# Kernel tuning notes

Hardware: AMD Instinct MI355X
Metric: run time of the kernel (lower is better)

The kernel has to match this reference:

```python
import jax, jax.numpy as jnp
import numpy as np

N_NODES = 40000
N_EDGES = 640000
D_IN = 128
D_OUT = 128
ALPHA = 0.5   # real-valued complex alpha from init
Q = 0.25      # magnetic potential parameter


def setup_inputs() -> dict:
    key = jax.random.key(0)
    k = jax.random.split(key, 6)
    x = jax.random.normal(k[0], (N_NODES, D_IN), dtype=jnp.float32)
    edge_index = jax.random.randint(k[1], (2, N_EDGES), 0, N_NODES, dtype=jnp.int32)
    W1 = jax.random.normal(k[2], (D_IN, D_OUT), dtype=jnp.float32) * 0.05
    b1 = jax.random.normal(k[3], (D_OUT,), dtype=jnp.float32) * 0.05
    W2 = jax.random.normal(k[4], (D_IN, D_OUT), dtype=jnp.float32) * 0.05
    b2 = jax.random.normal(k[5], (D_OUT,), dtype=jnp.float32) * 0.05
    return {"x": x, "edge_index": edge_index, "W1": W1, "b1": b1, "W2": W2, "b2": b2}


def _magnet_spmm(x, edge_index, q):
    """y = H @ x where H = D_s^{-1/2} (A_s * exp(i*2*pi*q*(A - A^T))) D_s^{-1/2},
    A_s = 0.5*(A + A^T). Returns (y_real, y_imag); x is real (zero imag part)."""
    n = x.shape[0]
    row, col = edge_index[0], edge_index[1]
    e = row.shape[0]
    # detect whether the reverse edge (col,row) exists in the edge set
    keys = row * n + col
    rkeys = col * n + row
    sk = jnp.sort(keys)
    pos = jnp.searchsorted(sk, rkeys)
    has_rev = (pos < e) & (sk[jnp.clip(pos, 0, e - 1)] == rkeys)
    # symmetrize: each directed edge contributes 0.5 in both directions.
    # forward copy carries phase sign +1, reversed copy sign -1; phase is 0
    # when both directions exist (A - A^T = 0 there).
    r_all = jnp.concatenate([row, col])          # [2E]
    c_all = jnp.concatenate([col, row])
    sign = jnp.concatenate([jnp.ones((e,), x.dtype), -jnp.ones((e,), x.dtype)])
    hr = jnp.concatenate([has_rev, has_rev]).astype(x.dtype)
    theta = (2.0 * np.pi * q) * sign * (1.0 - hr)
    half = jnp.asarray(0.5, x.dtype)
    # symmetrized degree: deg[u] = sum_v A_s[u,v]
    deg = jax.ops.segment_sum(jnp.full((2 * e,), 0.5, x.dtype), r_all, num_segments=n)
    dinv = jnp.where(deg > 0, 1.0 / jnp.sqrt(deg), 0.0)
    scale = half * dinv[r_all] * dinv[c_all]
    val_re = scale * jnp.cos(theta)
    val_im = scale * jnp.sin(theta)
    xg = x[c_all]                                # [2E, D] gather
    y_re = jax.ops.segment_sum(val_re[:, None] * xg, r_all, num_segments=n)
    y_im = jax.ops.segment_sum(val_im[:, None] * xg, r_all, num_segments=n)
    return y_re, y_im


def reference(x, edge_index, W1, b1, W2, b2):
    y_re, y_im = _magnet_spmm(x, edge_index, Q)
    # alpha * lin1(y) + (1-alpha) * lin2(y), applied to real and imag parts
    out_re = ALPHA * (y_re @ W1 + b1) + (1.0 - ALPHA) * (y_re @ W2 + b2)
    out_im = ALPHA * (y_im @ W1 + b1) + (1.0 - ALPHA) * (y_im @ W2 + b2)
    return jnp.concatenate([out_re, out_im], axis=1)  # [N, 2*D_OUT]
```

## Files before the change

kernel.cpp:

```cpp
#include <hip/hip_runtime.h>
#include <math.h>

#define N_NODES 40000
#define D 128
#define NEDGE 640000
#define CAP 80
#define ZNB 64

__device__ __forceinline__ unsigned short bf16rn(float f) {
    unsigned u = __float_as_uint(f);
    unsigned r = u + 0x7FFFu + ((u >> 16) & 1u);
    return (unsigned short)(r >> 16);
}

__global__ __launch_bounds__(256) void zgemm_kernel(
    const float* __restrict__ x, const float* __restrict__ W1, const float* __restrict__ W2,
    unsigned short* __restrict__ z, int* __restrict__ cursorA, int* __restrict__ cursorB) {
    int tid = threadIdx.x;
    int gtid = blockIdx.x * 256 + tid;
    int gstride = gridDim.x * 256;
    for (int t = gtid; t < N_NODES; t += gstride) { cursorA[t] = 0; cursorB[t] = 0; }

    __shared__ float xl[ZNB][129];
    int node0 = blockIdx.x * ZNB;
    const float4* xs = (const float4*)(x + (size_t)node0 * D);
    for (int t = tid; t < ZNB * (D / 4); t += 256)
        *(float4*)&xl[t >> 5][(t & 31) * 4] = xs[t];
    __syncthreads();

    int ng = tid >> 4;
    int c8 = tid & 15;
    float acc[4][8];
    #pragma unroll
    for (int q = 0; q < 4; ++q)
        #pragma unroll
        for (int j = 0; j < 8; ++j) acc[q][j] = 0.f;

    const float4* W1v = (const float4*)W1;
    const float4* W2v = (const float4*)W2;
    #pragma unroll 2
    for (int k = 0; k < D; ++k) {
        float4 a1 = W1v[k * 32 + c8 * 2],     u1 = W1v[k * 32 + c8 * 2 + 1];
        float4 a2 = W2v[k * 32 + c8 * 2],     u2 = W2v[k * 32 + c8 * 2 + 1];
        float w[8];
        w[0] = 0.5f * (a1.x + a2.x); w[1] = 0.5f * (a1.y + a2.y);
        w[2] = 0.5f * (a1.z + a2.z); w[3] = 0.5f * (a1.w + a2.w);
        w[4] = 0.5f * (u1.x + u2.x); w[5] = 0.5f * (u1.y + u2.y);
        w[6] = 0.5f * (u1.z + u2.z); w[7] = 0.5f * (u1.w + u2.w);
        #pragma unroll
        for (int q = 0; q < 4; ++q) {
            float xv = xl[ng * 4 + q][k];
            #pragma unroll
            for (int j = 0; j < 8; ++j) acc[q][j] += xv * w[j];
        }
    }
    #pragma unroll
    for (int q = 0; q < 4; ++q) {
        int node = node0 + ng * 4 + q;
        ushort4 o1, o2;
        o1.x = bf16rn(acc[q][0]); o1.y = bf16rn(acc[q][1]);
        o1.z = bf16rn(acc[q][2]); o1.w = bf16rn(acc[q][3]);
        o2.x = bf16rn(acc[q][4]); o2.y = bf16rn(acc[q][5]);
        o2.z = bf16rn(acc[q][6]); o2.w = bf16rn(acc[q][7]);
        ushort4* zp = (ushort4*)(z + (size_t)node * D + c8 * 8);
        zp[0] = o1; zp[1] = o2;
    }
}

__global__ void expand_kernel(const int* __restrict__ row, const int* __restrict__ col,
                              int* __restrict__ cursorA, int* __restrict__ cursorB,
                              unsigned short* __restrict__ entries) {
    int i = blockIdx.x * blockDim.x + threadIdx.x;
    int gstride = gridDim.x * blockDim.x;
    for (int e = i; e < NEDGE; e += gstride) {
        int r = row[e], c = col[e];
        int p1 = atomicAdd(&cursorA[r], 1);
        if (p1 < CAP) entries[(size_t)r * CAP + p1] = (unsigned short)c;
        int p2 = atomicAdd(&cursorB[c], 1);
        if (p2 < CAP) entries[(size_t)c * CAP + (CAP - 1 - p2)] = (unsigned short)r;
    }
}

__global__ __launch_bounds__(256) void gather_kernel(
    const unsigned short* __restrict__ z, const unsigned short* __restrict__ entries,
    const int* __restrict__ cursorA, const int* __restrict__ cursorB,
    const float* __restrict__ b1, const float* __restrict__ b2,
    float* __restrict__ out) {
    __shared__ unsigned short rawlds[4][2][CAP];
    __shared__ uint2 slds[4][2][CAP];

    int tid = threadIdx.x;
    int wave = tid >> 6, half = (tid >> 5) & 1, l = tid & 31;
    int n = wave * 2 + half;
    int u = blockIdx.x * 8 + n;

    int cA = cursorA[u], cB = cursorB[u];
    int a = min(cA, CAP);
    int b = min(cB, CAP - a);
    int m = a + b;
    int cnt = cA + cB;
    float dinv_u = (cnt > 0) ? rsqrtf(0.5f * (float)cnt) : 0.f;
    const unsigned short* eb = entries + (size_t)u * CAP;
    int gap = CAP - m;

    for (int t = l; t < m; t += 32)
        rawlds[wave][half][t] = eb[t < a ? t : t + gap];
    __builtin_amdgcn_wave_barrier();

    for (int t = l; t < m; t += 32) {
        unsigned short src = rawlds[wave][half][t];
        bool d1 = (t >= a);
        int lo = d1 ? 0 : a, hi = d1 ? a : m;
        bool rev = false;
        for (int j = lo; j < hi; ++j)
            rev |= (rawlds[wave][half][j] == src);
        int cs = cursorA[src] + cursorB[src];
        float s = 0.5f * dinv_u * rsqrtf(0.5f * (float)max(cs, 1));
        unsigned flag = 0u;
        float sval;
        if (rev) { sval = s; flag = 0x10000u; }
        else     { sval = d1 ? -s : s; }
        slds[wave][half][t] = make_uint2((unsigned)src | flag, __float_as_uint(sval));
    }
    __builtin_amdgcn_wave_barrier();

    float4 accre = make_float4(0.f, 0.f, 0.f, 0.f);
    float4 accim = make_float4(0.f, 0.f, 0.f, 0.f);

    #pragma unroll 8
    for (int i = 0; i < m; ++i) {
        uint2 t = slds[wave][half][i];
        unsigned src = t.x & 0xFFFFu;
        float s = __uint_as_float(t.y);
        bool isre = (t.x & 0x10000u) != 0u;
        float fre = isre ? s : 0.f;
        float fim = isre ? 0.f : s;
        uint2 v = ((const uint2*)(z + (size_t)src * D))[l];
        float v0 = __uint_as_float(v.x << 16);
        float v1 = __uint_as_float(v.x & 0xFFFF0000u);
        float v2 = __uint_as_float(v.y << 16);
        float v3 = __uint_as_float(v.y & 0xFFFF0000u);
        accre.x += fre * v0; accre.y += fre * v1;
        accre.z += fre * v2; accre.w += fre * v3;
        accim.x += fim * v0; accim.y += fim * v1;
        accim.z += fim * v2; accim.w += fim * v3;
    }

    float4 ba = ((const float4*)b1)[l];
    float4 bb = ((const float4*)b2)[l];
    float4 bv = make_float4(0.5f * (ba.x + bb.x), 0.5f * (ba.y + bb.y),
                            0.5f * (ba.z + bb.z), 0.5f * (ba.w + bb.w));
    accre.x += bv.x; accre.y += bv.y; accre.z += bv.z; accre.w += bv.w;
    accim.x += bv.x; accim.y += bv.y; accim.z += bv.z; accim.w += bv.w;

    *(float4*)&out[(size_t)u * 256 + l * 4] = accre;
    *(float4*)&out[(size_t)u * 256 + 128 + l * 4] = accim;
}

extern "C" void kernel_launch(void* const* d_in, const int* in_sizes, int n_in,
                              void* d_out, int out_size, void* d_ws, size_t ws_size,
                              hipStream_t stream) {
    const float* x  = (const float*)d_in[0];
    const int*   ei = (const int*)d_in[1];
    const float* W1 = (const float*)d_in[2];
    const float* b1 = (const float*)d_in[3];
    const float* W2 = (const float*)d_in[4];
    const float* b2 = (const float*)d_in[5];
    float* out = (float*)d_out;
    const int* row = ei;
    const int* col = ei + NEDGE;

    char* ws = (char*)d_ws;
    int*            cursorA = (int*)ws;
    int*            cursorB = (int*)(ws + 160000);
    unsigned short* entries = (unsigned short*)(ws + 320000);
    unsigned short* z       = (unsigned short*)(ws + 6720000);

    zgemm_kernel<<<N_NODES / ZNB, 256, 0, stream>>>(x, W1, W2, z, cursorA, cursorB);
    expand_kernel<<<2500, 256, 0, stream>>>(row, col, cursorA, cursorB, entries);
    gather_kernel<<<N_NODES / 8, 256, 0, stream>>>(z, entries, cursorA, cursorB, b1, b2, out);
}
```

Before: 201.5 us.

## Merge edge expansion and node GEMM into one heterogeneous launch with padded cursors

Splits work into an init kernel that zeroes cursors and precombines W1/W2 and b1/b2, then a single work kernel whose first blocks do the atomic edge bucketing while the remaining blocks compute the bf16 node projection, so the two phases can overlap. Cursors are packed as (a,b) pairs padded to 64 bytes, giving one int2 load per node and spreading atomics across cache lines. The GEMM drops its LDS-tiled 4x8 register blocking for a simpler one-node-per-32-threads loop, which re-reads x and W from global/cache and may lower compute efficiency. Padding makes the cursor array much larger to zero and gather.

```diff
diff --git a/kernel.cpp b/kernel.cpp
--- a/kernel.cpp
+++ b/kernel.cpp
@@ -5,7 +5,10 @@
 #define D 128
 #define NEDGE 640000
 #define CAP 80
-#define ZNB 64
+#define EB 2500
+#define ZB 5000
+
+struct Cur { int a; int b; int pad[14]; };
 
 __device__ __forceinline__ unsigned short bf16rn(float f) {
     unsigned u = __float_as_uint(f);
@@ -13,79 +16,57 @@
     return (unsigned short)(r >> 16);
 }
 
-__global__ __launch_bounds__(256) void zgemm_kernel(
-    const float* __restrict__ x, const float* __restrict__ W1, const float* __restrict__ W2,
-    unsigned short* __restrict__ z, int* __restrict__ cursorA, int* __restrict__ cursorB) {
-    int tid = threadIdx.x;
-    int gtid = blockIdx.x * 256 + tid;
-    int gstride = gridDim.x * 256;
-    for (int t = gtid; t < N_NODES; t += gstride) { cursorA[t] = 0; cursorB[t] = 0; }
-
-    __shared__ float xl[ZNB][129];
-    int node0 = blockIdx.x * ZNB;
-    const float4* xs = (const float4*)(x + (size_t)node0 * D);
-    for (int t = tid; t < ZNB * (D / 4); t += 256)
-        *(float4*)&xl[t >> 5][(t & 31) * 4] = xs[t];
-    __syncthreads();
-
-    int ng = tid >> 4;
-    int c8 = tid & 15;
-    float acc[4][8];
-    #pragma unroll
-    for (int q = 0; q < 4; ++q)
-        #pragma unroll
-        for (int j = 0; j < 8; ++j) acc[q][j] = 0.f;
-
-    const float4* W1v = (const float4*)W1;
-    const float4* W2v = (const float4*)W2;
-    #pragma unroll 2
-    for (int k = 0; k < D; ++k) {
-        float4 a1 = W1v[k * 32 + c8 * 2],     u1 = W1v[k * 32 + c8 * 2 + 1];
-        float4 a2 = W2v[k * 32 + c8 * 2],     u2 = W2v[k * 32 + c8 * 2 + 1];
-        float w[8];
-        w[0] = 0.5f * (a1.x + a2.x); w[1] = 0.5f * (a1.y + a2.y);
-        w[2] = 0.5f * (a1.z + a2.z); w[3] = 0.5f * (a1.w + a2.w);
-        w[4] = 0.5f * (u1.x + u2.x); w[5] = 0.5f * (u1.y + u2.y);
-        w[6] = 0.5f * (u1.z + u2.z); w[7] = 0.5f * (u1.w + u2.w);
-        #pragma unroll
-        for (int q = 0; q < 4; ++q) {
-            float xv = xl[ng * 4 + q][k];
-            #pragma unroll
-            for (int j = 0; j < 8; ++j) acc[q][j] += xv * w[j];
-        }
-    }
-    #pragma unroll
-    for (int q = 0; q < 4; ++q) {
-        int node = node0 + ng * 4 + q;
-        ushort4 o1, o2;
-        o1.x = bf16rn(acc[q][0]); o1.y = bf16rn(acc[q][1]);
-        o1.z = bf16rn(acc[q][2]); o1.w = bf16rn(acc[q][3]);
-        o2.x = bf16rn(acc[q][4]); o2.y = bf16rn(acc[q][5]);
-        o2.z = bf16rn(acc[q][6]); o2.w = bf16rn(acc[q][7]);
-        ushort4* zp = (ushort4*)(z + (size_t)node * D + c8 * 8);
-        zp[0] = o1; zp[1] = o2;
-    }
+__global__ void init_kernel(Cur* __restrict__ cur,
+                            const float* __restrict__ W1, const float* __restrict__ b1,
+                            const float* __restrict__ W2, const float* __restrict__ b2,
+                            float* __restrict__ Wc, float* __restrict__ bc) {
+    int i = blockIdx.x * blockDim.x + threadIdx.x;
+    int stride = gridDim.x * blockDim.x;
+    uint4* cz = (uint4*)cur;
+    uint4 zero = make_uint4(0u, 0u, 0u, 0u);
+    for (int t = i; t < N_NODES * 4; t += stride) cz[t] = zero;
+    for (int t = i; t < D * D; t += stride) Wc[t] = 0.5f * (W1[t] + W2[t]);
+    if (i < D) bc[i] = 0.5f * (b1[i] + b2[i]);
 }
 
-__global__ void expand_kernel(const int* __restrict__ row, const int* __restrict__ col,
-                              int* __restrict__ cursorA, int* __restrict__ cursorB,
-                              unsigned short* __restrict__ entries) {
-    int i = blockIdx.x * blockDim.x + threadIdx.x;
-    int gstride = gridDim.x * blockDim.x;
-    for (int e = i; e < NEDGE; e += gstride) {
+__global__ __launch_bounds__(256) void work_kernel(
+    const int* __restrict__ row, const int* __restrict__ col,
+    Cur* __restrict__ cur, unsigned short* __restrict__ entries,
+    const float* __restrict__ x, const float* __restrict__ Wc,
+    unsigned short* __restrict__ z) {
+    int bid = blockIdx.x;
+    int tid = threadIdx.x;
+    if (bid < EB) {
+        int e = bid * 256 + tid;
         int r = row[e], c = col[e];
-        int p1 = atomicAdd(&cursorA[r], 1);
+        int p1 = atomicAdd(&cur[r].a, 1);
         if (p1 < CAP) entries[(size_t)r * CAP + p1] = (unsigned short)c;
-        int p2 = atomicAdd(&cursorB[c], 1);
+        int p2 = atomicAdd(&cur[c].b, 1);
         if (p2 < CAP) entries[(size_t)c * CAP + (CAP - 1 - p2)] = (unsigned short)r;
+    } else {
+        int node = (bid - EB) * 8 + (tid >> 5);
+        int c4 = tid & 31;
+        const float* xr = x + (size_t)node * D;
+        const float4* Wv = (const float4*)Wc;
+        float4 acc = make_float4(0.f, 0.f, 0.f, 0.f);
+        #pragma unroll 4
+        for (int k = 0; k < D; ++k) {
+            float xv = xr[k];
+            float4 w = Wv[k * 32 + c4];
+            acc.x += xv * w.x; acc.y += xv * w.y;
+            acc.z += xv * w.z; acc.w += xv * w.w;
+        }
+        ushort4 o;
+        o.x = bf16rn(acc.x); o.y = bf16rn(acc.y);
+        o.z = bf16rn(acc.z); o.w = bf16rn(acc.w);
+        ((ushort4*)(z + (size_t)node * D))[c4] = o;
     }
 }
 
 __global__ __launch_bounds__(256) void gather_kernel(
     const unsigned short* __restrict__ z, const unsigned short* __restrict__ entries,
-    const int* __restrict__ cursorA, const int* __restrict__ cursorB,
-    const float* __restrict__ b1, const float* __restrict__ b2,
-    float* __restrict__ out) {
+    const Cur* __restrict__ cur,
+    const float* __restrict__ bc, float* __restrict__ out) {
     __shared__ unsigned short rawlds[4][2][CAP];
     __shared__ uint2 slds[4][2][CAP];
 
@@ -94,7 +75,8 @@
     int n = wave * 2 + half;
     int u = blockIdx.x * 8 + n;
 
-    int cA = cursorA[u], cB = cursorB[u];
+    int2 abU = *(const int2*)&cur[u];
+    int cA = abU.x, cB = abU.y;
     int a = min(cA, CAP);
     int b = min(cB, CAP - a);
     int m = a + b;
@@ -114,7 +96,8 @@
         bool rev = false;
         for (int j = lo; j < hi; ++j)
             rev |= (rawlds[wave][half][j] == src);
-        int cs = cursorA[src] + cursorB[src];
+        int2 abS = *(const int2*)&cur[src];
+        int cs = abS.x + abS.y;
         float s = 0.5f * dinv_u * rsqrtf(0.5f * (float)max(cs, 1));
         unsigned flag = 0u;
         float sval;
@@ -146,10 +129,7 @@
         accim.z += fim * v2; accim.w += fim * v3;
     }
 
-    float4 ba = ((const float4*)b1)[l];
-    float4 bb = ((const float4*)b2)[l];
-    float4 bv = make_float4(0.5f * (ba.x + bb.x), 0.5f * (ba.y + bb.y),
-                            0.5f * (ba.z + bb.z), 0.5f * (ba.w + bb.w));
+    float4 bv = ((const float4*)bc)[l];
     accre.x += bv.x; accre.y += bv.y; accre.z += bv.z; accre.w += bv.w;
     accim.x += bv.x; accim.y += bv.y; accim.z += bv.z; accim.w += bv.w;
 
@@ -171,12 +151,13 @@
     const int* col = ei + NEDGE;
 
     char* ws = (char*)d_ws;
-    int*            cursorA = (int*)ws;
-    int*            cursorB = (int*)(ws + 160000);
-    unsigned short* entries = (unsigned short*)(ws + 320000);
-    unsigned short* z       = (unsigned short*)(ws + 6720000);
+    float*          Wc      = (float*)ws;
+    float*          bc      = (float*)(ws + 65536);
+    Cur*            cur     = (Cur*)(ws + 66048);
+    unsigned short* entries = (unsigned short*)(ws + 2626048);
+    unsigned short* z       = (unsigned short*)(ws + 9026048);
 
-    zgemm_kernel<<<N_NODES / ZNB, 256, 0, stream>>>(x, W1, W2, z, cursorA, cursorB);
-    expand_kernel<<<2500, 256, 0, stream>>>(row, col, cursorA, cursorB, entries);
-    gather_kernel<<<N_NODES / 8, 256, 0, stream>>>(z, entries, cursorA, cursorB, b1, b2, out);
+    init_kernel<<<512, 256, 0, stream>>>(cur, W1, b1, W2, b2, Wc, bc);
+    work_kernel<<<EB + ZB, 256, 0, stream>>>(row, col, cur, entries, x, Wc, z);
+    gather_kernel<<<N_NODES / 8, 256, 0, stream>>>(z, entries, cur, bc, out);
 }
```

Result: slower. 251.2 us (+24.6%).
